# Optimization experiments

Hardware: AMD Instinct MI355X
Metric: run time of the kernel (lower is better)

## Reference

```python
import jax, jax.numpy as jnp
import numpy as np

S = 2048       # seq_len
D = 1024       # d_model
H = 16         # heads
DK = 64        # d_k = d_v = D // H


def setup_inputs() -> dict:
    key = jax.random.key(0)
    ks = jax.random.split(key, 12)
    sc_in = 1.0 / np.sqrt(D)
    return {
        "Q": jax.random.normal(ks[0], (S, D), jnp.float32),
        "K": jax.random.normal(ks[1], (S, D), jnp.float32),
        "V": jax.random.normal(ks[2], (S, D), jnp.float32),
        # stacked per-head projection weights (torch Linear math: x @ W + b, W stored [in,out])
        "Wq": jax.random.normal(ks[3], (H, D, DK), jnp.float32) * sc_in,
        "bq": jnp.zeros((H, DK), jnp.float32),
        "Wk": jax.random.normal(ks[4], (H, D, DK), jnp.float32) * sc_in,
        "bk": jnp.zeros((H, DK), jnp.float32),
        "Wv": jax.random.normal(ks[5], (H, D, DK), jnp.float32) * sc_in,
        "bv": jnp.zeros((H, DK), jnp.float32),
        "Wo": jax.random.normal(ks[6], (H * DK, D), jnp.float32) * (1.0 / np.sqrt(H * DK)),
        "bo": jnp.zeros((D,), jnp.float32),
    }


def reference(Q, K, V, Wq, bq, Wk, bk, Wv, bv, Wo, bo):
    # per-head projections, all heads at once: [S,D] x [H,D,DK] -> [H,S,DK]
    q = jnp.einsum("sd,hdk->hsk", Q, Wq) + bq[:, None, :]
    k = jnp.einsum("sd,hdk->hsk", K, Wk) + bk[:, None, :]
    v = jnp.einsum("sd,hdk->hsk", V, Wv) + bv[:, None, :]
    # scaled dot-product attention per head: [H,S,S]
    scores = jnp.einsum("hsk,htk->hst", q, k) / jnp.sqrt(jnp.asarray(DK, q.dtype))
    attn = jax.nn.softmax(scores, axis=-1)
    heads = jnp.einsum("hst,htv->hsv", attn, v)          # [H,S,DK]
    concat = heads.transpose(1, 0, 2).reshape(S, H * DK)  # [S, H*DK]
    return concat @ Wo + bo                               # [S, D]
```

## Files before the change

kernel.cpp:

```cpp
#include <hip/hip_runtime.h>
#include <stdint.h>

#define S_LEN 2048
#define D_MODEL 1024
#define NH 16
#define DKV 64

typedef unsigned short u16;
typedef __bf16 bf16x8 __attribute__((ext_vector_type(8)));
typedef float f32x4 __attribute__((ext_vector_type(4)));

__device__ __forceinline__ u16 f2bf(float f) {
  union { float f; uint32_t u; } v; v.f = f;
  uint32_t r = v.u + 0x7FFFu + ((v.u >> 16) & 1u);
  return (u16)(r >> 16);
}
__device__ __forceinline__ uint32_t pkbf(float lo, float hi) {
  union { float f; uint32_t u; } a, b; a.f = lo; b.f = hi;
  return ((b.u + 0x8000u) & 0xFFFF0000u) | ((a.u + 0x8000u) >> 16);
}
__device__ __forceinline__ void gl16(const u16* g, u16* l) {
  __builtin_amdgcn_global_load_lds(
      (const __attribute__((address_space(1))) unsigned int*)g,
      (__attribute__((address_space(3))) unsigned int*)l, 16, 0, 0);
}

__global__ __launch_bounds__(256) void prep_k(
    const float* __restrict__ Q, const float* __restrict__ K,
    const float* __restrict__ V, const float* __restrict__ Wq,
    const float* __restrict__ Wk, const float* __restrict__ Wv,
    const float* __restrict__ Wo, u16* __restrict__ QKVb,
    u16* __restrict__ Wqt, u16* __restrict__ Wkt, u16* __restrict__ Wvt,
    u16* __restrict__ Wot) {
  __shared__ float tile[32][33];
  const int idx = blockIdx.x;
  if (idx < 6144) {
    const int z = idx >> 11, blk = idx & 2047;
    const float* src = (z == 0) ? Q : (z == 1) ? K : V;
    u16* dst = QKVb + (size_t)z * S_LEN * D_MODEL;
    size_t i = ((size_t)blk * 256 + threadIdx.x) * 4;
    const float4 v = *(const float4*)(src + i);
    union { u16 h[4]; uint2 u2; } o;
    o.h[0] = f2bf(v.x); o.h[1] = f2bf(v.y); o.h[2] = f2bf(v.z); o.h[3] = f2bf(v.w);
    *(uint2*)(dst + i) = o.u2;
    return;
  }
  const float* ip; u16* op; int R, C, r0, c0;
  if (idx < 9216) {
    int t = idx - 6144;
    int which = t >> 10, head = (t & 1023) >> 6, tl = t & 63;
    ip = ((which == 0) ? Wq : (which == 1) ? Wk : Wv) + (size_t)head * D_MODEL * DKV;
    op = ((which == 0) ? Wqt : (which == 1) ? Wkt : Wvt) + (size_t)head * D_MODEL * DKV;
    R = D_MODEL; C = DKV; c0 = (tl & 1) * 32; r0 = (tl >> 1) * 32;
  } else {
    int t = idx - 9216;
    ip = Wo; op = Wot; R = D_MODEL; C = D_MODEL;
    c0 = (t & 31) * 32; r0 = (t >> 5) * 32;
  }
  int tr = threadIdx.x >> 5, tc = threadIdx.x & 31;
#pragma unroll
  for (int i = 0; i < 4; i++)
    tile[tr + i * 8][tc] = ip[(size_t)(r0 + tr + i * 8) * C + c0 + tc];
  __syncthreads();
#pragma unroll
  for (int i = 0; i < 4; i++) {
    int c = tr + i * 8;
    op[(size_t)(c0 + c) * R + r0 + tc] = f2bf(tile[tc][c]);
  }
}

__global__ __launch_bounds__(256, 2) void proj_gemm_k(
    const u16* __restrict__ qkvb, const u16* __restrict__ Wqt,
    const u16* __restrict__ Wkt, const u16* __restrict__ Wvt,
    const float* __restrict__ bq, const float* __restrict__ bk,
    const float* __restrict__ bv,
    u16* __restrict__ qb, u16* __restrict__ kb, u16* __restrict__ vT) {
  const int bid = blockIdx.x;
  const int l = (bid & 7) * 96 + (bid >> 3);
  const int z = l >> 8, rem = l & 255;
  const int m0 = (rem >> 4) * 128, n0 = (rem & 15) * 64;
  const u16* A = qkvb + (size_t)z * S_LEN * D_MODEL;
  const u16* Bt = (z == 0) ? Wqt : (z == 1) ? Wkt : Wvt;
  const float* bias = (z == 0) ? bq : (z == 1) ? bk : bv;
  const float scale = (z == 0) ? 0.18033688f : 1.0f;

  __shared__ __align__(16) u16 smem[36864];
  const int tid = threadIdx.x;
  const int w = tid >> 6, lane = tid & 63, quad = lane >> 4, l15 = lane & 15;
  const int wm = (w >> 1) * 64, wn = (w & 1) * 32;
  const int pbA = w * 256, pbB = w * 128;

  f32x4 acc[4][2] = {};

  {
#pragma unroll
    for (int b = 0; b < 2; b++) {
      const int k0 = b * 64;
      u16* As = smem + b * 8192;
      u16* Bs = smem + 24576 + b * 4096;
#pragma unroll
      for (int e = 0; e < 4; e++) {
        int p = pbA + e * 64 + lane;
        int r = p >> 3, cg = (p & 7) ^ (r & 7);
        gl16(&A[(size_t)(m0 + r) * D_MODEL + k0 + cg * 8], As + (pbA + e * 64) * 8);
      }
#pragma unroll
      for (int e = 0; e < 2; e++) {
        int p = pbB + e * 64 + lane;
        int r = p >> 3, cg = (p & 7) ^ (r & 7);
        gl16(&Bt[(size_t)(n0 + r) * D_MODEL + k0 + cg * 8], Bs + (pbB + e * 64) * 8);
      }
    }
  }
#pragma unroll
  for (int it = 0; it < 16; it++) {
    const int rd = it % 3;
    if (it < 15) asm volatile("s_waitcnt vmcnt(6)" ::: "memory");
    else         asm volatile("s_waitcnt vmcnt(0)" ::: "memory");
    __builtin_amdgcn_s_barrier();
    __builtin_amdgcn_sched_barrier(0);
    if (it < 14) {
      const int wr = (rd + 2) % 3;
      const int k0 = (it + 2) * 64;
      u16* As = smem + wr * 8192;
      u16* Bs = smem + 24576 + wr * 4096;
#pragma unroll
      for (int e = 0; e < 4; e++) {
        int p = pbA + e * 64 + lane;
        int r = p >> 3, cg = (p & 7) ^ (r & 7);
        gl16(&A[(size_t)(m0 + r) * D_MODEL + k0 + cg * 8], As + (pbA + e * 64) * 8);
      }
#pragma unroll
      for (int e = 0; e < 2; e++) {
        int p = pbB + e * 64 + lane;
        int r = p >> 3, cg = (p & 7) ^ (r & 7);
        gl16(&Bt[(size_t)(n0 + r) * D_MODEL + k0 + cg * 8], Bs + (pbB + e * 64) * 8);
      }
    }
    const u16* As = smem + rd * 8192;
    const u16* Bs = smem + 24576 + rd * 4096;
#pragma unroll
    for (int kc = 0; kc < 2; kc++) {
      bf16x8 af[4], bfr[2];
      const int c = kc * 4 + quad;
#pragma unroll
      for (int t = 0; t < 4; t++) {
        int ma = wm + t * 16 + l15;
        af[t] = *(const bf16x8*)&As[(ma * 8 + (c ^ (ma & 7))) * 8];
      }
#pragma unroll
      for (int t = 0; t < 2; t++) {
        int na = wn + t * 16 + l15;
        bfr[t] = *(const bf16x8*)&Bs[(na * 8 + (c ^ (na & 7))) * 8];
      }
      __builtin_amdgcn_s_setprio(1);
#pragma unroll
      for (int tm = 0; tm < 4; tm++)
#pragma unroll
        for (int tn = 0; tn < 2; tn++)
          acc[tm][tn] = __builtin_amdgcn_mfma_f32_16x16x32_bf16(af[tm], bfr[tn], acc[tm][tn], 0, 0, 0);
      __builtin_amdgcn_s_setprio(0);
    }
  }

  if (z < 2) {
    u16* O = (z == 0) ? qb : kb;
#pragma unroll
    for (int tm = 0; tm < 4; tm++)
#pragma unroll
      for (int tn = 0; tn < 2; tn++)
#pragma unroll
        for (int r = 0; r < 4; r++) {
          int row = m0 + wm + tm * 16 + quad * 4 + r;
          int col = n0 + wn + tn * 16 + l15;
          O[(size_t)row * D_MODEL + col] = f2bf((acc[tm][tn][r] + bias[col]) * scale);
        }
  } else {
#pragma unroll
    for (int tm = 0; tm < 4; tm++)
#pragma unroll
      for (int tn = 0; tn < 2; tn++) {
        int col = n0 + wn + tn * 16 + l15;
        int row0 = m0 + wm + tm * 16 + quad * 4;
        float b = bias[col];
        union { u16 h[4]; uint2 u2; } o;
#pragma unroll
        for (int r = 0; r < 4; r++) o.h[r] = f2bf(acc[tm][tn][r] + b);
        *(uint2*)&vT[(size_t)col * S_LEN + row0] = o.u2;
      }
  }
}

__global__ __launch_bounds__(512) void attn_k(
    const u16* __restrict__ qb, const u16* __restrict__ kb,
    const u16* __restrict__ vT, u16* __restrict__ conc) {
  const int bid = blockIdx.x;
  const int l = (bid & 7) * 64 + (bid >> 3);
  const int h = l >> 5, qblk = (l & 31) * 64;
  const int tid = threadIdx.x;
  const int w = tid >> 6, lane = tid & 63, quad = lane >> 4, l15 = lane & 15;
  const int half = w >> 2, wq = w & 3;
  const int q0 = qblk + wq * 16;

  __shared__ __align__(16) u16 smem[39936];
  u16* Kh = smem + half * 8192;
  u16* Vh = smem + 16384 + half * 8192;
  u16* Pw = smem + 32768 + w * 896;

  bf16x8 qf[2];
#pragma unroll
  for (int kc = 0; kc < 2; kc++)
    qf[kc] = *(const bf16x8*)&qb[(size_t)(q0 + l15) * D_MODEL + h * 64 + kc * 32 + quad * 8];

  const u16* kbase = kb + (size_t)h * 64;
  const u16* vbase = vT + (size_t)(h * 64) * S_LEN;

  const int p = wq * 64 + lane;
  const int kr = p >> 3, kcg = (p & 7) ^ (kr & 7);
  const int vr = p >> 2, vcg = (p & 3) ^ (vr & 3);
  const size_t kgoff = (size_t)kr * D_MODEL + kcg * 8;
  const size_t vgoff = (size_t)vr * S_LEN + vcg * 8;
  const int ldsoff = wq * 64 * 8;

  f32x4 oacc[4] = {};
  float lsum = 0.f;

  {
#pragma unroll
    for (int s = 0; s < 3; s++) {
      const int t0 = half * 1024 + s * 32;
      gl16(kbase + (size_t)t0 * D_MODEL + kgoff, Kh + s * 2048 + ldsoff);
      gl16(vbase + t0 + vgoff, Vh + s * 2048 + ldsoff);
    }
  }

#pragma unroll
  for (int it = 0; it < 32; it++) {
    const int rd = it & 3;
    if (it < 30)       asm volatile("s_waitcnt vmcnt(4)" ::: "memory");
    else if (it == 30) asm volatile("s_waitcnt vmcnt(2)" ::: "memory");
    else               asm volatile("s_waitcnt vmcnt(0)" ::: "memory");
    __builtin_amdgcn_s_barrier();
    __builtin_amdgcn_sched_barrier(0);
    if (it < 29) {
      const int wr = (it + 3) & 3;
      const int t0n = half * 1024 + (it + 3) * 32;
      gl16(kbase + (size_t)t0n * D_MODEL + kgoff, Kh + wr * 2048 + ldsoff);
      gl16(vbase + t0n + vgoff, Vh + wr * 2048 + ldsoff);
    }
    const u16* Kc = Kh + rd * 2048;
    const u16* Vc = Vh + rd * 2048;

    f32x4 sacc[2] = {};
    __builtin_amdgcn_s_setprio(1);
#pragma unroll
    for (int kc = 0; kc < 2; kc++)
#pragma unroll
      for (int tn = 0; tn < 2; tn++) {
        int rr = tn * 16 + l15;
        bf16x8 ka = *(const bf16x8*)&Kc[(rr * 8 + ((kc * 4 + quad) ^ (rr & 7))) * 8];
        sacc[tn] = __builtin_amdgcn_mfma_f32_16x16x32_bf16(ka, qf[kc], sacc[tn], 0, 0, 0);
      }
    __builtin_amdgcn_s_setprio(0);

#pragma unroll
    for (int tn = 0; tn < 2; tn++) {
      float p0 = __builtin_amdgcn_exp2f(sacc[tn][0]);
      float p1 = __builtin_amdgcn_exp2f(sacc[tn][1]);
      float p2 = __builtin_amdgcn_exp2f(sacc[tn][2]);
      float p3 = __builtin_amdgcn_exp2f(sacc[tn][3]);
      lsum += (p0 + p1) + (p2 + p3);
      uint2 pw2; pw2.x = pkbf(p0, p1); pw2.y = pkbf(p2, p3);
      *(uint2*)&Pw[l15 * 56 + tn * 16 + quad * 4] = pw2;
    }

    bf16x8 pa = *(const bf16x8*)&Pw[l15 * 56 + quad * 8];
    __builtin_amdgcn_s_setprio(1);
#pragma unroll
    for (int nt = 0; nt < 4; nt++) {
      int dv = nt * 16 + l15;
      bf16x8 vb = *(const bf16x8*)&Vc[(dv * 4 + (quad ^ (dv & 3))) * 8];
      oacc[nt] = __builtin_amdgcn_mfma_f32_16x16x32_bf16(pa, vb, oacc[nt], 0, 0, 0);
    }
    __builtin_amdgcn_s_setprio(0);
  }
  __syncthreads();

  lsum += __shfl_xor(lsum, 16, 64);
  lsum += __shfl_xor(lsum, 32, 64);

  float* OshF = (float*)smem;
  float* lshF = OshF + 8 * 16 * 68;
  if (lane < 16) lshF[w * 16 + lane] = lsum;
#pragma unroll
  for (int nt = 0; nt < 4; nt++)
#pragma unroll
    for (int r = 0; r < 4; r++)
      OshF[w * 1088 + (quad * 4 + r) * 68 + nt * 16 + l15] = oacc[nt][r];
  __syncthreads();

  const int q = tid >> 3;
  const int dv0 = (tid & 7) * 8;
  const int wa = q >> 4, wb = wa + 4, qr = q & 15;
  const float* pa = &OshF[wa * 1088 + qr * 68 + dv0];
  const float* pb = &OshF[wb * 1088 + qr * 68 + dv0];
  float4 a0 = *(const float4*)pa, a1 = *(const float4*)(pa + 4);
  float4 b0 = *(const float4*)pb, b1 = *(const float4*)(pb + 4);
  float li = 1.0f / (lshF[wa * 16 + qr] + lshF[wb * 16 + qr]);
  union { u16 hh[8]; uint4 u4; } o;
  o.hh[0] = f2bf((a0.x + b0.x) * li); o.hh[1] = f2bf((a0.y + b0.y) * li);
  o.hh[2] = f2bf((a0.z + b0.z) * li); o.hh[3] = f2bf((a0.w + b0.w) * li);
  o.hh[4] = f2bf((a1.x + b1.x) * li); o.hh[5] = f2bf((a1.y + b1.y) * li);
  o.hh[6] = f2bf((a1.z + b1.z) * li); o.hh[7] = f2bf((a1.w + b1.w) * li);
  *(uint4*)&conc[(size_t)(qblk + q) * D_MODEL + h * 64 + dv0] = o.u4;
}

__global__ __launch_bounds__(256, 2) void out_gemm_k(
    const u16* __restrict__ A, const u16* __restrict__ Bt,
    const float* __restrict__ bias, float* __restrict__ out) {
  const int bid = blockIdx.x;
  const int l = (bid & 7) * 64 + (bid >> 3);
  const int m0 = (l >> 4) * 64, n0 = (l & 15) * 64;
  __shared__ __align__(16) u16 smem[8 * 4096];
  const int tid = threadIdx.x;
  const int w = tid >> 6, lane = tid & 63, quad = lane >> 4, l15 = lane & 15;
  const int wm = (w >> 1) * 32, wn = (w & 1) * 32;
  const int pb = w * 128;

  f32x4 acc[2][2] = {};
  {
#pragma unroll
    for (int s = 0; s < 3; s++) {
      const int k0 = s * 64;
#pragma unroll
      for (int e = 0; e < 2; e++) {
        int p = pb + e * 64 + lane;
        int r = p >> 3, cg = (p & 7) ^ (r & 7);
        gl16(&A[(size_t)(m0 + r) * D_MODEL + k0 + cg * 8], smem + s * 4096 + (pb + e * 64) * 8);
        gl16(&Bt[(size_t)(n0 + r) * D_MODEL + k0 + cg * 8], smem + 16384 + s * 4096 + (pb + e * 64) * 8);
      }
    }
  }
#pragma unroll
  for (int it = 0; it < 16; it++) {
    const int rd = it & 3;
    if (it < 14)       asm volatile("s_waitcnt vmcnt(8)" ::: "memory");
    else if (it == 14) asm volatile("s_waitcnt vmcnt(4)" ::: "memory");
    else               asm volatile("s_waitcnt vmcnt(0)" ::: "memory");
    __builtin_amdgcn_s_barrier();
    __builtin_amdgcn_sched_barrier(0);
    if (it < 13) {
      const int wr = (it + 3) & 3;
      const int k0 = (it + 3) * 64;
      u16* As = smem + wr * 4096;
      u16* Bs = smem + 16384 + wr * 4096;
#pragma unroll
      for (int e = 0; e < 2; e++) {
        int p = pb + e * 64 + lane;
        int r = p >> 3, cg = (p & 7) ^ (r & 7);
        gl16(&A[(size_t)(m0 + r) * D_MODEL + k0 + cg * 8], As + (pb + e * 64) * 8);
        gl16(&Bt[(size_t)(n0 + r) * D_MODEL + k0 + cg * 8], Bs + (pb + e * 64) * 8);
      }
    }
    const u16* As = smem + rd * 4096;
    const u16* Bs = smem + 16384 + rd * 4096;
#pragma unroll
    for (int kc = 0; kc < 2; kc++) {
      const int c = kc * 4 + quad;
      bf16x8 af[2], bfr[2];
#pragma unroll
      for (int t = 0; t < 2; t++) {
        int ma = wm + t * 16 + l15, na = wn + t * 16 + l15;
        af[t] = *(const bf16x8*)&As[(ma * 8 + (c ^ (ma & 7))) * 8];
        bfr[t] = *(const bf16x8*)&Bs[(na * 8 + (c ^ (na & 7))) * 8];
      }
      __builtin_amdgcn_s_setprio(1);
#pragma unroll
      for (int tm = 0; tm < 2; tm++)
#pragma unroll
        for (int tn = 0; tn < 2; tn++)
          acc[tm][tn] = __builtin_amdgcn_mfma_f32_16x16x32_bf16(af[tm], bfr[tn], acc[tm][tn], 0, 0, 0);
      __builtin_amdgcn_s_setprio(0);
    }
  }
#pragma unroll
  for (int tm = 0; tm < 2; tm++)
#pragma unroll
    for (int tn = 0; tn < 2; tn++)
#pragma unroll
      for (int r = 0; r < 4; r++) {
        int row = m0 + wm + tm * 16 + quad * 4 + r;
        int col = n0 + wn + tn * 16 + l15;
        out[(size_t)row * D_MODEL + col] = acc[tm][tn][r] + bias[col];
      }
}

extern "C" void kernel_launch(void* const* d_in, const int* in_sizes, int n_in,
                              void* d_out, int out_size, void* d_ws, size_t ws_size,
                              hipStream_t stream) {
  const float* Q  = (const float*)d_in[0];
  const float* K  = (const float*)d_in[1];
  const float* V  = (const float*)d_in[2];
  const float* Wq = (const float*)d_in[3];
  const float* bq = (const float*)d_in[4];
  const float* Wk = (const float*)d_in[5];
  const float* bk = (const float*)d_in[6];
  const float* Wv = (const float*)d_in[7];
  const float* bv = (const float*)d_in[8];
  const float* Wo = (const float*)d_in[9];
  const float* bo = (const float*)d_in[10];
  float* out = (float*)d_out;

  u16* ws = (u16*)d_ws;
  u16* QKVb = ws;
  u16* Wqt  = QKVb + (size_t)3 * S_LEN * D_MODEL;
  u16* Wkt  = Wqt + (size_t)D_MODEL * D_MODEL;
  u16* Wvt  = Wkt + (size_t)D_MODEL * D_MODEL;
  u16* Wot  = Wvt + (size_t)D_MODEL * D_MODEL;
  u16* qbuf = Wot + (size_t)D_MODEL * D_MODEL;
  u16* kbuf = qbuf + (size_t)S_LEN * D_MODEL;
  u16* vTb  = kbuf + (size_t)S_LEN * D_MODEL;
  u16* conc = vTb + (size_t)S_LEN * D_MODEL;

  prep_k<<<dim3(10240), 256, 0, stream>>>(Q, K, V, Wq, Wk, Wv, Wo,
                                          QKVb, Wqt, Wkt, Wvt, Wot);
  proj_gemm_k<<<dim3(768), 256, 0, stream>>>(
      QKVb, Wqt, Wkt, Wvt, bq, bk, bv, qbuf, kbuf, vTb);
  attn_k<<<dim3(512), 512, 0, stream>>>(qbuf, kbuf, vTb, conc);
  out_gemm_k<<<dim3(512), 256, 0, stream>>>(conc, Wot, bo, out);
}
```

Baseline: 154.2 us.

## Software-pipeline attention loop: overlap PV MFMA of previous tile with QK of current

Restructures the attention inner loop so the P·V MFMAs for the previous key tile are issued right after the QK^T MFMAs for the current tile, letting exp2/softmax work overlap with matrix-core work. V loads are staggered one iteration behind K loads, with adjusted vmcnt waits, and a drain step after the loop handles the last tile. The aim is to hide exp/pack latency and LDS round-trip stalls between the two GEMMs, at the cost of more complex wait accounting and an extra barrier at the end.

```diff
diff --git a/kernel.cpp b/kernel.cpp
--- a/kernel.cpp
+++ b/kernel.cpp
@@ -226,33 +226,34 @@
   float lsum = 0.f;
 
   {
-#pragma unroll
-    for (int s = 0; s < 3; s++) {
-      const int t0 = half * 1024 + s * 32;
-      gl16(kbase + (size_t)t0 * D_MODEL + kgoff, Kh + s * 2048 + ldsoff);
-      gl16(vbase + t0 + vgoff, Vh + s * 2048 + ldsoff);
-    }
+    const int t0 = half * 1024;
+    gl16(kbase + (size_t)(t0 + 0) * D_MODEL + kgoff, Kh + 0 * 2048 + ldsoff);
+    gl16(kbase + (size_t)(t0 + 32) * D_MODEL + kgoff, Kh + 1 * 2048 + ldsoff);
+    gl16(vbase + (t0 + 0) + vgoff, Vh + 0 * 2048 + ldsoff);
+    gl16(kbase + (size_t)(t0 + 64) * D_MODEL + kgoff, Kh + 2 * 2048 + ldsoff);
+    gl16(vbase + (t0 + 32) + vgoff, Vh + 1 * 2048 + ldsoff);
   }
 
 #pragma unroll
   for (int it = 0; it < 32; it++) {
     const int rd = it & 3;
     if (it < 30)       asm volatile("s_waitcnt vmcnt(4)" ::: "memory");
-    else if (it == 30) asm volatile("s_waitcnt vmcnt(2)" ::: "memory");
-    else               asm volatile("s_waitcnt vmcnt(0)" ::: "memory");
+    else if (it == 30) asm volatile("s_waitcnt vmcnt(3)" ::: "memory");
+    else               asm volatile("s_waitcnt vmcnt(1)" ::: "memory");
     __builtin_amdgcn_s_barrier();
     __builtin_amdgcn_sched_barrier(0);
     if (it < 29) {
-      const int wr = (it + 3) & 3;
       const int t0n = half * 1024 + (it + 3) * 32;
-      gl16(kbase + (size_t)t0n * D_MODEL + kgoff, Kh + wr * 2048 + ldsoff);
-      gl16(vbase + t0n + vgoff, Vh + wr * 2048 + ldsoff);
+      gl16(kbase + (size_t)t0n * D_MODEL + kgoff, Kh + ((it + 3) & 3) * 2048 + ldsoff);
+    }
+    if (it < 30) {
+      const int t0v = half * 1024 + (it + 2) * 32;
+      gl16(vbase + t0v + vgoff, Vh + ((it + 2) & 3) * 2048 + ldsoff);
     }
     const u16* Kc = Kh + rd * 2048;
-    const u16* Vc = Vh + rd * 2048;
-
+
+    __builtin_amdgcn_s_setprio(1);
     f32x4 sacc[2] = {};
-    __builtin_amdgcn_s_setprio(1);
 #pragma unroll
     for (int kc = 0; kc < 2; kc++)
 #pragma unroll
@@ -261,6 +262,16 @@
         bf16x8 ka = *(const bf16x8*)&Kc[(rr * 8 + ((kc * 4 + quad) ^ (rr & 7))) * 8];
         sacc[tn] = __builtin_amdgcn_mfma_f32_16x16x32_bf16(ka, qf[kc], sacc[tn], 0, 0, 0);
       }
+    if (it > 0) {
+      const u16* Vc = Vh + ((it - 1) & 3) * 2048;
+      bf16x8 pa = *(const bf16x8*)&Pw[l15 * 56 + quad * 8];
+#pragma unroll
+      for (int nt = 0; nt < 4; nt++) {
+        int dv = nt * 16 + l15;
+        bf16x8 vb = *(const bf16x8*)&Vc[(dv * 4 + (quad ^ (dv & 3))) * 8];
+        oacc[nt] = __builtin_amdgcn_mfma_f32_16x16x32_bf16(pa, vb, oacc[nt], 0, 0, 0);
+      }
+    }
     __builtin_amdgcn_s_setprio(0);
 
 #pragma unroll
@@ -273,16 +284,19 @@
       uint2 pw2; pw2.x = pkbf(p0, p1); pw2.y = pkbf(p2, p3);
       *(uint2*)&Pw[l15 * 56 + tn * 16 + quad * 4] = pw2;
     }
-
+  }
+  asm volatile("s_waitcnt vmcnt(0)" ::: "memory");
+  __builtin_amdgcn_s_barrier();
+  __builtin_amdgcn_sched_barrier(0);
+  {
+    const u16* Vc = Vh + (31 & 3) * 2048;
     bf16x8 pa = *(const bf16x8*)&Pw[l15 * 56 + quad * 8];
-    __builtin_amdgcn_s_setprio(1);
 #pragma unroll
     for (int nt = 0; nt < 4; nt++) {
       int dv = nt * 16 + l15;
       bf16x8 vb = *(const bf16x8*)&Vc[(dv * 4 + (quad ^ (dv & 3))) * 8];
       oacc[nt] = __builtin_amdgcn_mfma_f32_16x16x32_bf16(pa, vb, oacc[nt], 0, 0, 0);
     }
-    __builtin_amdgcn_s_setprio(0);
   }
   __syncthreads();
 
```

After: 156.2 us. Within noise of the previous version (+1.3%).

## Load K/V attention fragments directly from global into registers, dropping LDS staging

Applied to the files above, without the earlier changes.

Replaces the LDS ring buffer fed by async global-to-LDS loads and per-iteration barriers with per-wave register double-buffering of K and V MFMA fragments loaded straight from global memory. This removes block-wide barriers, LDS traffic and shared memory footprint, which could raise occupancy. In exchange each wave fetches the same K/V tiles independently, multiplying global/L2 traffic, and the loads are less coalesced.

```diff
diff --git a/kernel.cpp b/kernel.cpp
--- a/kernel.cpp
+++ b/kernel.cpp
@@ -202,65 +202,55 @@
   const int half = w >> 2, wq = w & 3;
   const int q0 = qblk + wq * 16;
 
-  __shared__ __align__(16) u16 smem[39936];
-  u16* Kh = smem + half * 8192;
-  u16* Vh = smem + 16384 + half * 8192;
-  u16* Pw = smem + 32768 + w * 896;
+  __shared__ __align__(16) u16 smem[24832];
+  u16* Pw = smem + 17664 + w * 896;
 
   bf16x8 qf[2];
 #pragma unroll
   for (int kc = 0; kc < 2; kc++)
     qf[kc] = *(const bf16x8*)&qb[(size_t)(q0 + l15) * D_MODEL + h * 64 + kc * 32 + quad * 8];
 
-  const u16* kbase = kb + (size_t)h * 64;
-  const u16* vbase = vT + (size_t)(h * 64) * S_LEN;
-
-  const int p = wq * 64 + lane;
-  const int kr = p >> 3, kcg = (p & 7) ^ (kr & 7);
-  const int vr = p >> 2, vcg = (p & 3) ^ (vr & 3);
-  const size_t kgoff = (size_t)kr * D_MODEL + kcg * 8;
-  const size_t vgoff = (size_t)vr * S_LEN + vcg * 8;
-  const int ldsoff = wq * 64 * 8;
+  const u16* klp = kb + (size_t)(half * 1024 + l15) * D_MODEL + h * 64 + quad * 8;
+  const u16* vlp = vT + (size_t)(h * 64 + l15) * S_LEN + half * 1024 + quad * 8;
 
   f32x4 oacc[4] = {};
   float lsum = 0.f;
 
+  bf16x8 kfr[2][4], vfr[2][4];
   {
 #pragma unroll
-    for (int s = 0; s < 3; s++) {
-      const int t0 = half * 1024 + s * 32;
-      gl16(kbase + (size_t)t0 * D_MODEL + kgoff, Kh + s * 2048 + ldsoff);
-      gl16(vbase + t0 + vgoff, Vh + s * 2048 + ldsoff);
-    }
+    for (int i = 0; i < 4; i++) {
+      const int kc = i >> 1, tn = i & 1;
+      kfr[0][i] = *(const bf16x8*)(klp + (size_t)(tn * 16) * D_MODEL + kc * 32);
+    }
+#pragma unroll
+    for (int nt = 0; nt < 4; nt++)
+      vfr[0][nt] = *(const bf16x8*)(vlp + (size_t)(nt * 16) * S_LEN);
   }
 
 #pragma unroll
   for (int it = 0; it < 32; it++) {
-    const int rd = it & 3;
-    if (it < 30)       asm volatile("s_waitcnt vmcnt(4)" ::: "memory");
-    else if (it == 30) asm volatile("s_waitcnt vmcnt(2)" ::: "memory");
-    else               asm volatile("s_waitcnt vmcnt(0)" ::: "memory");
-    __builtin_amdgcn_s_barrier();
-    __builtin_amdgcn_sched_barrier(0);
-    if (it < 29) {
-      const int wr = (it + 3) & 3;
-      const int t0n = half * 1024 + (it + 3) * 32;
-      gl16(kbase + (size_t)t0n * D_MODEL + kgoff, Kh + wr * 2048 + ldsoff);
-      gl16(vbase + t0n + vgoff, Vh + wr * 2048 + ldsoff);
-    }
-    const u16* Kc = Kh + rd * 2048;
-    const u16* Vc = Vh + rd * 2048;
+    const int cur = it & 1, nxt = cur ^ 1;
+    if (it < 31) {
+      const size_t ko = (size_t)((it + 1) * 32) * D_MODEL;
+      const int vo = (it + 1) * 32;
+#pragma unroll
+      for (int i = 0; i < 4; i++) {
+        const int kc = i >> 1, tn = i & 1;
+        kfr[nxt][i] = *(const bf16x8*)(klp + ko + (size_t)(tn * 16) * D_MODEL + kc * 32);
+      }
+#pragma unroll
+      for (int nt = 0; nt < 4; nt++)
+        vfr[nxt][nt] = *(const bf16x8*)(vlp + (size_t)(nt * 16) * S_LEN + vo);
+    }
 
     f32x4 sacc[2] = {};
     __builtin_amdgcn_s_setprio(1);
 #pragma unroll
     for (int kc = 0; kc < 2; kc++)
 #pragma unroll
-      for (int tn = 0; tn < 2; tn++) {
-        int rr = tn * 16 + l15;
-        bf16x8 ka = *(const bf16x8*)&Kc[(rr * 8 + ((kc * 4 + quad) ^ (rr & 7))) * 8];
-        sacc[tn] = __builtin_amdgcn_mfma_f32_16x16x32_bf16(ka, qf[kc], sacc[tn], 0, 0, 0);
-      }
+      for (int tn = 0; tn < 2; tn++)
+        sacc[tn] = __builtin_amdgcn_mfma_f32_16x16x32_bf16(kfr[cur][kc * 2 + tn], qf[kc], sacc[tn], 0, 0, 0);
     __builtin_amdgcn_s_setprio(0);
 
 #pragma unroll
@@ -277,14 +267,10 @@
     bf16x8 pa = *(const bf16x8*)&Pw[l15 * 56 + quad * 8];
     __builtin_amdgcn_s_setprio(1);
 #pragma unroll
-    for (int nt = 0; nt < 4; nt++) {
-      int dv = nt * 16 + l15;
-      bf16x8 vb = *(const bf16x8*)&Vc[(dv * 4 + (quad ^ (dv & 3))) * 8];
-      oacc[nt] = __builtin_amdgcn_mfma_f32_16x16x32_bf16(pa, vb, oacc[nt], 0, 0, 0);
-    }
+    for (int nt = 0; nt < 4; nt++)
+      oacc[nt] = __builtin_amdgcn_mfma_f32_16x16x32_bf16(pa, vfr[cur][nt], oacc[nt], 0, 0, 0);
     __builtin_amdgcn_s_setprio(0);
   }
-  __syncthreads();
 
   lsum += __shfl_xor(lsum, 16, 64);
   lsum += __shfl_xor(lsum, 32, 64);
```

Result: slower. 240.7 us (+56.1%).
